# Performance work log

Measured on AMD Instinct MI355X. Metric: run time of the kernel, lower is better.

## Reference

```python
import jax, jax.numpy as jnp
import numpy as np

IN_F, OUT_F = 512, 512
GRID_SIZE, SPLINE_ORDER = 5, 3
K = GRID_SIZE + SPLINE_ORDER  # 8 basis functions
B, S = 8, 1024


def setup_inputs() -> dict:
    key = jax.random.key(0)
    k1, k2, k3, k4, k5 = jax.random.split(key, 5)
    return {
        "x": jax.random.normal(k1, (B, S, IN_F), dtype=jnp.float32),
        "coeff": jax.random.normal(k2, (OUT_F, IN_F, K), dtype=jnp.float32),
        "scale_base": jax.random.normal(k3, (OUT_F, IN_F), dtype=jnp.float32) * 0.1,
        "scale_spline": jax.random.normal(k4, (OUT_F, IN_F), dtype=jnp.float32),
        "base_bias": jax.random.normal(k5, (OUT_F, IN_F), dtype=jnp.float32),
    }


def reference(x, coeff, scale_base, scale_spline, base_bias):
    batch = x.shape[0]
    in_f = x.shape[-1]
    k = coeff.shape[-1]

    xc = jnp.clip(x.reshape(-1, in_f), -1.0, 1.0)      # (N, in)
    base = jax.nn.silu(xc)                              # (N, in)

    # polynomial basis recurrence: b0 = 1, b1 = x, b_i = 2*x*b_{i-1} - 1
    bases = [jnp.ones_like(xc), xc]
    for _ in range(2, k):
        bases.append(2.0 * xc * bases[-1] - 1.0)
    basis = jnp.stack(bases[:k], axis=-1)               # (N, in, K)

    # spline[n,o] = sum_{i,k} scale_spline[o,i]*coeff[o,i,k]*basis[n,i,k]
    w_spline = scale_spline[..., None] * coeff          # (out, in, K)
    spline_term = jnp.einsum('nik,oik->no', basis, w_spline)
    base_term = base @ scale_base.T                     # (N, out)
    out = base_term + spline_term + jnp.sum(base_bias, axis=1)  # (N, out)

    out = out.reshape(batch, -1, base_bias.shape[0])    # (B, S, out)
    if out.shape[-2] == 1:
        out = out[..., 0, :]
    return out
```

## Files before the change

kernel.cpp:

```cpp
#include <hip/hip_runtime.h>
#include <hip/hip_bf16.h>

#define IN_FEAT 512
#define OUT_FEAT 512
#define NTOK 8192
#define KDIM 4096

typedef short bf16x8 __attribute__((ext_vector_type(8)));
typedef float f32x16 __attribute__((ext_vector_type(16)));

static __device__ inline short f2bf(float f) {
    union { float f; unsigned u; } v; v.f = f;
    unsigned u = v.u;
    u += 0x7fffu + ((u >> 16) & 1u);
    return (short)(u >> 16);
}

static __device__ inline unsigned cvtpk(float lo, float hi) {
    unsigned r;
    asm("v_cvt_pk_bf16_f32 %0, %1, %2" : "=v"(r) : "v"(lo), "v"(hi));
    return r;
}

static __device__ inline bf16x8 gen_chunk(float xv) {
    float xc = fminf(fmaxf(xv, -1.f), 1.f);
    float e  = __expf(-xc);
    float bse = xc * __builtin_amdgcn_rcpf(1.f + e);
    float b2 = 2.f * xc * xc - 1.f;
    float b3 = 2.f * xc * b2 - 1.f;
    float b4 = 2.f * xc * b3 - 1.f;
    float b5 = 2.f * xc * b4 - 1.f;
    float b6 = 2.f * xc * b5 - 1.f;
    float b7 = 2.f * xc * b6 - 1.f;
    union { uint4 u; bf16x8 v; } r;
    r.u.x = cvtpk(bse, xc);
    r.u.y = cvtpk(b2, b3);
    r.u.z = cvtpk(b4, b5);
    r.u.w = cvtpk(b6, b7);
    return r.v;
}

static __device__ inline void gload_lds16(const short* g, short* l) {
    __builtin_amdgcn_global_load_lds(
        (const __attribute__((address_space(1))) unsigned int*)g,
        (__attribute__((address_space(3))) unsigned int*)l,
        16, 0, 0);
}

__global__ __launch_bounds__(256) void kan_prep(
    const float* __restrict__ coeff, const float* __restrict__ scale_base,
    const float* __restrict__ scale_spline, const float* __restrict__ base_bias,
    short* __restrict__ Wb, float* __restrict__ bias)
{
    int o = blockIdx.x;
    int tid = threadIdx.x;
    float local = 0.f;
#pragma unroll
    for (int rep = 0; rep < 2; ++rep) {
        int i = tid + rep * 256;
        size_t oi = (size_t)o * IN_FEAT + i;
        const float4* c4 = (const float4*)(coeff + oi * 8);
        float4 ca = c4[0], cb = c4[1];
        float ss = scale_spline[oi];
        float sb = scale_base[oi];
        local += base_bias[oi] + ss * ca.x;
        bf16x8 w;
        w[0] = f2bf(sb);
        w[1] = f2bf(ss * ca.y); w[2] = f2bf(ss * ca.z); w[3] = f2bf(ss * ca.w);
        w[4] = f2bf(ss * cb.x); w[5] = f2bf(ss * cb.y); w[6] = f2bf(ss * cb.z);
        w[7] = f2bf(ss * cb.w);
        *(bf16x8*)(Wb + (size_t)o * KDIM + (size_t)i * 8) = w;
    }
    __shared__ float red[4];
    for (int off = 32; off > 0; off >>= 1) local += __shfl_down(local, off, 64);
    int lane = tid & 63, wv = tid >> 6;
    if (lane == 0) red[wv] = local;
    __syncthreads();
    if (tid == 0) bias[o] = red[0] + red[1] + red[2] + red[3];
}

__global__ __launch_bounds__(256, 2) void kan_gemm16(
    const float* __restrict__ x, const short* __restrict__ Wb,
    const float* __restrict__ bias, float* __restrict__ out)
{
    __shared__ __align__(16) short POOL[20480];
    short* Bs = POOL;

    int tid = threadIdx.x;
    int nb = blockIdx.x & 7;
    int mb = blockIdx.x >> 3;
    int m0 = mb * 128, o0 = nb * 64;

    int lane = tid & 63, wv = tid >> 6;
    int kk = wv;
    int l31 = lane & 31, half = lane >> 5;
    int rm  = l31 & 15;

    f32x16 acc[4][2];
#pragma unroll
    for (int a = 0; a < 4; ++a)
#pragma unroll
        for (int b = 0; b < 2; ++b) acc[a][b] = (f32x16)0.f;

    int rl = lane >> 4, q = lane & 15;
    const short* pB0 = Wb + (size_t)(o0 + wv * 16 +  0 + rl) * KDIM + (size_t)(q ^ ( 0 + rl)) * 8;
    const short* pB1 = Wb + (size_t)(o0 + wv * 16 +  4 + rl) * KDIM + (size_t)(q ^ ( 4 + rl)) * 8;
    const short* pB2 = Wb + (size_t)(o0 + wv * 16 +  8 + rl) * KDIM + (size_t)(q ^ ( 8 + rl)) * 8;
    const short* pB3 = Wb + (size_t)(o0 + wv * 16 + 12 + rl) * KDIM + (size_t)(q ^ (12 + rl)) * 8;

    const float* xp0 = x + (size_t)(m0 + l31) * IN_FEAT + kk * 4;

    int s0 = kk * 4 + half, s1 = s0 + 2;
    int of00 = l31 * 128        + ((s0 ^ rm) * 8);
    int of01 = (32 + l31) * 128 + ((s0 ^ rm) * 8);
    int of10 = l31 * 128        + ((s1 ^ rm) * 8);
    int of11 = (32 + l31) * 128 + ((s1 ^ rm) * 8);

#define MFMA_(A, B, C) __builtin_amdgcn_mfma_f32_32x32x16_bf16(A, B, C, 0, 0, 0)

#define STAGE(BUF, IT, P0, P1, P2, P3)                                        \
    {                                                                         \
        short* bd_ = Bs + (BUF) * 8192 + wv * 2048;                           \
        const size_t bo_ = (size_t)(IT) * 128;                                \
        gload_lds16(pB0 + bo_, bd_);                                          \
        gload_lds16(pB1 + bo_, bd_ + 512);                                    \
        gload_lds16(pB2 + bo_, bd_ + 1024);                                   \
        gload_lds16(pB3 + bo_, bd_ + 1536);                                   \
        const float* xq_ = xp0 + (size_t)(IT) * 16;                           \
        P0 = *(const float4*)(xq_);                                           \
        P1 = *(const float4*)(xq_ + 16384);                                   \
        P2 = *(const float4*)(xq_ + 32768);                                   \
        P3 = *(const float4*)(xq_ + 49152);                                   \
    }

#define COMPUTE(CUR, P0, P1, P2, P3)                                          \
    {                                                                         \
        const short* Bsc_ = Bs + (CUR) * 8192;                                \
        bf16x8 b00 = *(const bf16x8*)(Bsc_ + of00);                           \
        bf16x8 b01 = *(const bf16x8*)(Bsc_ + of01);                           \
        bf16x8 b10 = *(const bf16x8*)(Bsc_ + of10);                           \
        bf16x8 b11 = *(const bf16x8*)(Bsc_ + of11);                           \
        bf16x8 a0 = gen_chunk(half ? (P0).y : (P0).x);                        \
        bf16x8 a1 = gen_chunk(half ? (P1).y : (P1).x);                        \
        bf16x8 a2 = gen_chunk(half ? (P2).y : (P2).x);                        \
        bf16x8 a3 = gen_chunk(half ? (P3).y : (P3).x);                        \
        acc[0][0] = MFMA_(a0, b00, acc[0][0]); acc[0][1] = MFMA_(a0, b01, acc[0][1]); \
        acc[1][0] = MFMA_(a1, b00, acc[1][0]); acc[1][1] = MFMA_(a1, b01, acc[1][1]); \
        acc[2][0] = MFMA_(a2, b00, acc[2][0]); acc[2][1] = MFMA_(a2, b01, acc[2][1]); \
        acc[3][0] = MFMA_(a3, b00, acc[3][0]); acc[3][1] = MFMA_(a3, b01, acc[3][1]); \
        a0 = gen_chunk(half ? (P0).w : (P0).z);                               \
        a1 = gen_chunk(half ? (P1).w : (P1).z);                               \
        a2 = gen_chunk(half ? (P2).w : (P2).z);                               \
        a3 = gen_chunk(half ? (P3).w : (P3).z);                               \
        acc[0][0] = MFMA_(a0, b10, acc[0][0]); acc[0][1] = MFMA_(a0, b11, acc[0][1]); \
        acc[1][0] = MFMA_(a1, b10, acc[1][0]); acc[1][1] = MFMA_(a1, b11, acc[1][1]); \
        acc[2][0] = MFMA_(a2, b10, acc[2][0]); acc[2][1] = MFMA_(a2, b11, acc[2][1]); \
        acc[3][0] = MFMA_(a3, b10, acc[3][0]); acc[3][1] = MFMA_(a3, b11, acc[3][1]); \
    }

    float4 Pa0, Pa1, Pa2, Pa3, Pb0, Pb1, Pb2, Pb3;

    STAGE(0, 0, Pa0, Pa1, Pa2, Pa3);
    for (int j = 0; j < 16; ++j) {
        const int e = 2 * j;
        __syncthreads();
        STAGE(1, e + 1, Pb0, Pb1, Pb2, Pb3);
        COMPUTE(0, Pa0, Pa1, Pa2, Pa3);
        __syncthreads();
        if (e + 1 < 31) STAGE(0, e + 2, Pa0, Pa1, Pa2, Pa3);
        COMPUTE(1, Pb0, Pb1, Pb2, Pb3);
    }
#undef STAGE
#undef COMPUTE
#undef MFMA_

    float* rbuf = (float*)POOL;
#pragma unroll
    for (int p = 0; p < 2; ++p) {
        __syncthreads();
        if (kk >= 2) {
            float* s_ = rbuf + (size_t)(kk - 2) * 4224 + lane * 66;
#pragma unroll
            for (int fm = 0; fm < 2; ++fm)
#pragma unroll
                for (int fn = 0; fn < 2; ++fn)
#pragma unroll
                    for (int r = 0; r < 16; ++r)
                        s_[(fm * 2 + fn) * 16 + r] = acc[2 * p + fm][fn][r];
        }
        __syncthreads();
        if (kk < 2) {
            const float* s_ = rbuf + (size_t)kk * 4224 + lane * 66;
#pragma unroll
            for (int fm = 0; fm < 2; ++fm)
#pragma unroll
                for (int fn = 0; fn < 2; ++fn)
#pragma unroll
                    for (int r = 0; r < 16; ++r)
                        acc[2 * p + fm][fn][r] += s_[(fm * 2 + fn) * 16 + r];
        }
        __syncthreads();
        if (kk == 1) {
            float* s_ = rbuf + lane * 66;
#pragma unroll
            for (int fm = 0; fm < 2; ++fm)
#pragma unroll
                for (int fn = 0; fn < 2; ++fn)
#pragma unroll
                    for (int r = 0; r < 16; ++r)
                        s_[(fm * 2 + fn) * 16 + r] = acc[2 * p + fm][fn][r];
        }
        __syncthreads();
        if (kk == 0) {
            const float* s_ = rbuf + lane * 66;
#pragma unroll
            for (int fn = 0; fn < 2; ++fn) {
                int o = o0 + fn * 32 + l31;
                float bv = bias[o];
#pragma unroll
                for (int fm = 0; fm < 2; ++fm) {
#pragma unroll
                    for (int r = 0; r < 16; ++r) {
                        float v = acc[2 * p + fm][fn][r] + s_[(fm * 2 + fn) * 16 + r] + bv;
                        int token = m0 + (2 * p + fm) * 32 + (r & 3) + 8 * (r >> 2) + 4 * half;
                        out[(size_t)token * OUT_FEAT + o] = v;
                    }
                }
            }
        }
    }
}

extern "C" void kernel_launch(void* const* d_in, const int* in_sizes, int n_in,
                              void* d_out, int out_size, void* d_ws, size_t ws_size,
                              hipStream_t stream) {
    const float* x            = (const float*)d_in[0];
    const float* coeff        = (const float*)d_in[1];
    const float* scale_base   = (const float*)d_in[2];
    const float* scale_spline = (const float*)d_in[3];
    const float* base_bias    = (const float*)d_in[4];
    float* out = (float*)d_out;

    short* Wb   = (short*)d_ws;
    float* bias = (float*)((char*)d_ws + (size_t)OUT_FEAT * KDIM * 2);

    kan_prep<<<OUT_FEAT, 256, 0, stream>>>(coeff, scale_base, scale_spline, base_bias, Wb, bias);
    kan_gemm16<<<(NTOK / 128) * (OUT_FEAT / 64), 256, 0, stream>>>(x, Wb, bias, out);
}
```

Baseline: 127.9 us.

## Double K-step per stage and remap block order for L2 locality

Each pipeline stage now covers 256 K-elements instead of 128. That halves the iterations and the number of __syncthreads barriers, and the B tile in LDS grows to 64x256 with a 32-way XOR swizzle. Each COMPUTE now issues four sub-steps of MFMAs per stage. Block indices are also remapped so that groups of 8 consecutive blocks share N-tiles across M, aiming for better L2 reuse of x or W. The cost is more LDS (64KB) and more registers for prefetched x, which may hurt occupancy at 2 blocks per CU.

```diff
diff --git a/kernel.cpp b/kernel.cpp
--- a/kernel.cpp
+++ b/kernel.cpp
@@ -79,22 +79,23 @@
     if (tid == 0) bias[o] = red[0] + red[1] + red[2] + red[3];
 }
 
-__global__ __launch_bounds__(256, 2) void kan_gemm16(
+__global__ __launch_bounds__(256, 2) void kan_gemm17(
     const float* __restrict__ x, const short* __restrict__ Wb,
     const float* __restrict__ bias, float* __restrict__ out)
 {
-    __shared__ __align__(16) short POOL[20480];
+    __shared__ __align__(16) short POOL[32768];
     short* Bs = POOL;
 
     int tid = threadIdx.x;
-    int nb = blockIdx.x & 7;
-    int mb = blockIdx.x >> 3;
+    int bid = blockIdx.x;
+    int j8 = bid & 7, t = bid >> 3;
+    int mb = j8 * 8 + (t & 7);
+    int nb = t >> 3;
     int m0 = mb * 128, o0 = nb * 64;
 
     int lane = tid & 63, wv = tid >> 6;
     int kk = wv;
     int l31 = lane & 31, half = lane >> 5;
-    int rm  = l31 & 15;
 
     f32x16 acc[4][2];
 #pragma unroll
@@ -102,76 +103,78 @@
 #pragma unroll
         for (int b = 0; b < 2; ++b) acc[a][b] = (f32x16)0.f;
 
-    int rl = lane >> 4, q = lane & 15;
-    const short* pB0 = Wb + (size_t)(o0 + wv * 16 +  0 + rl) * KDIM + (size_t)(q ^ ( 0 + rl)) * 8;
-    const short* pB1 = Wb + (size_t)(o0 + wv * 16 +  4 + rl) * KDIM + (size_t)(q ^ ( 4 + rl)) * 8;
-    const short* pB2 = Wb + (size_t)(o0 + wv * 16 +  8 + rl) * KDIM + (size_t)(q ^ ( 8 + rl)) * 8;
-    const short* pB3 = Wb + (size_t)(o0 + wv * 16 + 12 + rl) * KDIM + (size_t)(q ^ (12 + rl)) * 8;
-
-    const float* xp0 = x + (size_t)(m0 + l31) * IN_FEAT + kk * 4;
-
-    int s0 = kk * 4 + half, s1 = s0 + 2;
-    int of00 = l31 * 128        + ((s0 ^ rm) * 8);
-    int of01 = (32 + l31) * 128 + ((s0 ^ rm) * 8);
-    int of10 = l31 * 128        + ((s1 ^ rm) * 8);
-    int of11 = (32 + l31) * 128 + ((s1 ^ rm) * 8);
+    int rl2 = lane >> 5, q32 = lane & 31;
+    const short* pB[8];
+#pragma unroll
+    for (int c = 0; c < 8; ++c) {
+        int row = wv * 16 + c * 2 + rl2;
+        int g = q32 ^ (row & 31);
+        pB[c] = Wb + (size_t)(o0 + row) * KDIM + (size_t)g * 8;
+    }
+    int bd0 = wv * 16 * 256;
+
+    const float* xp0 = x + (size_t)(m0 + l31) * IN_FEAT + kk * 8;
+
+    int ofr[4];
+#pragma unroll
+    for (int j = 0; j < 4; ++j)
+        ofr[j] = l31 * 256 + (((kk * 8 + 2 * j + half) ^ l31) * 8);
 
 #define MFMA_(A, B, C) __builtin_amdgcn_mfma_f32_32x32x16_bf16(A, B, C, 0, 0, 0)
 
-#define STAGE(BUF, IT, P0, P1, P2, P3)                                        \
+#define GENSEL(Qa, Qb, J) ((J) == 0 ? (half ? (Qa).y : (Qa).x)                \
+                         : (J) == 1 ? (half ? (Qa).w : (Qa).z)                \
+                         : (J) == 2 ? (half ? (Qb).y : (Qb).x)                \
+                                    : (half ? (Qb).w : (Qb).z))
+
+#define STAGE(BUF, IT, Q0a, Q0b, Q1a, Q1b, Q2a, Q2b, Q3a, Q3b)                \
     {                                                                         \
-        short* bd_ = Bs + (BUF) * 8192 + wv * 2048;                           \
-        const size_t bo_ = (size_t)(IT) * 128;                                \
-        gload_lds16(pB0 + bo_, bd_);                                          \
-        gload_lds16(pB1 + bo_, bd_ + 512);                                    \
-        gload_lds16(pB2 + bo_, bd_ + 1024);                                   \
-        gload_lds16(pB3 + bo_, bd_ + 1536);                                   \
-        const float* xq_ = xp0 + (size_t)(IT) * 16;                           \
-        P0 = *(const float4*)(xq_);                                           \
-        P1 = *(const float4*)(xq_ + 16384);                                   \
-        P2 = *(const float4*)(xq_ + 32768);                                   \
-        P3 = *(const float4*)(xq_ + 49152);                                   \
-    }
-
-#define COMPUTE(CUR, P0, P1, P2, P3)                                          \
+        short* bd_ = Bs + (BUF) * 16384 + bd0;                                \
+        const size_t bo_ = (size_t)(IT) * 256;                                \
+        _Pragma("unroll")                                                     \
+        for (int c_ = 0; c_ < 8; ++c_)                                        \
+            gload_lds16(pB[c_] + bo_, bd_ + c_ * 512);                        \
+        const float* xq_ = xp0 + (size_t)(IT) * 32;                           \
+        Q0a = *(const float4*)(xq_);          Q0b = *(const float4*)(xq_ + 4);          \
+        Q1a = *(const float4*)(xq_ + 16384);  Q1b = *(const float4*)(xq_ + 16388);      \
+        Q2a = *(const float4*)(xq_ + 32768);  Q2b = *(const float4*)(xq_ + 32772);      \
+        Q3a = *(const float4*)(xq_ + 49152);  Q3b = *(const float4*)(xq_ + 49156);      \
+    }
+
+#define COMPUTE(CUR, Q0a, Q0b, Q1a, Q1b, Q2a, Q2b, Q3a, Q3b)                  \
     {                                                                         \
-        const short* Bsc_ = Bs + (CUR) * 8192;                                \
-        bf16x8 b00 = *(const bf16x8*)(Bsc_ + of00);                           \
-        bf16x8 b01 = *(const bf16x8*)(Bsc_ + of01);                           \
-        bf16x8 b10 = *(const bf16x8*)(Bsc_ + of10);                           \
-        bf16x8 b11 = *(const bf16x8*)(Bsc_ + of11);                           \
-        bf16x8 a0 = gen_chunk(half ? (P0).y : (P0).x);                        \
-        bf16x8 a1 = gen_chunk(half ? (P1).y : (P1).x);                        \
-        bf16x8 a2 = gen_chunk(half ? (P2).y : (P2).x);                        \
-        bf16x8 a3 = gen_chunk(half ? (P3).y : (P3).x);                        \
-        acc[0][0] = MFMA_(a0, b00, acc[0][0]); acc[0][1] = MFMA_(a0, b01, acc[0][1]); \
-        acc[1][0] = MFMA_(a1, b00, acc[1][0]); acc[1][1] = MFMA_(a1, b01, acc[1][1]); \
-        acc[2][0] = MFMA_(a2, b00, acc[2][0]); acc[2][1] = MFMA_(a2, b01, acc[2][1]); \
-        acc[3][0] = MFMA_(a3, b00, acc[3][0]); acc[3][1] = MFMA_(a3, b01, acc[3][1]); \
-        a0 = gen_chunk(half ? (P0).w : (P0).z);                               \
-        a1 = gen_chunk(half ? (P1).w : (P1).z);                               \
-        a2 = gen_chunk(half ? (P2).w : (P2).z);                               \
-        a3 = gen_chunk(half ? (P3).w : (P3).z);                               \
-        acc[0][0] = MFMA_(a0, b10, acc[0][0]); acc[0][1] = MFMA_(a0, b11, acc[0][1]); \
-        acc[1][0] = MFMA_(a1, b10, acc[1][0]); acc[1][1] = MFMA_(a1, b11, acc[1][1]); \
-        acc[2][0] = MFMA_(a2, b10, acc[2][0]); acc[2][1] = MFMA_(a2, b11, acc[2][1]); \
-        acc[3][0] = MFMA_(a3, b10, acc[3][0]); acc[3][1] = MFMA_(a3, b11, acc[3][1]); \
-    }
-
-    float4 Pa0, Pa1, Pa2, Pa3, Pb0, Pb1, Pb2, Pb3;
-
-    STAGE(0, 0, Pa0, Pa1, Pa2, Pa3);
-    for (int j = 0; j < 16; ++j) {
-        const int e = 2 * j;
-        __syncthreads();
-        STAGE(1, e + 1, Pb0, Pb1, Pb2, Pb3);
-        COMPUTE(0, Pa0, Pa1, Pa2, Pa3);
-        __syncthreads();
-        if (e + 1 < 31) STAGE(0, e + 2, Pa0, Pa1, Pa2, Pa3);
-        COMPUTE(1, Pb0, Pb1, Pb2, Pb3);
+        const short* Bc_ = Bs + (CUR) * 16384;                                \
+        _Pragma("unroll")                                                     \
+        for (int j_ = 0; j_ < 4; ++j_) {                                      \
+            bf16x8 b0_ = *(const bf16x8*)(Bc_ + ofr[j_]);                     \
+            bf16x8 b1_ = *(const bf16x8*)(Bc_ + ofr[j_] + 8192);              \
+            bf16x8 a0_ = gen_chunk(GENSEL(Q0a, Q0b, j_));                     \
+            bf16x8 a1_ = gen_chunk(GENSEL(Q1a, Q1b, j_));                     \
+            bf16x8 a2_ = gen_chunk(GENSEL(Q2a, Q2b, j_));                     \
+            bf16x8 a3_ = gen_chunk(GENSEL(Q3a, Q3b, j_));                     \
+            acc[0][0] = MFMA_(a0_, b0_, acc[0][0]); acc[0][1] = MFMA_(a0_, b1_, acc[0][1]); \
+            acc[1][0] = MFMA_(a1_, b0_, acc[1][0]); acc[1][1] = MFMA_(a1_, b1_, acc[1][1]); \
+            acc[2][0] = MFMA_(a2_, b0_, acc[2][0]); acc[2][1] = MFMA_(a2_, b1_, acc[2][1]); \
+            acc[3][0] = MFMA_(a3_, b0_, acc[3][0]); acc[3][1] = MFMA_(a3_, b1_, acc[3][1]); \
+        }                                                                     \
+    }
+
+    float4 A0a, A0b, A1a, A1b, A2a, A2b, A3a, A3b;
+    float4 B0a, B0b, B1a, B1b, B2a, B2b, B3a, B3b;
+
+    STAGE(0, 0, A0a, A0b, A1a, A1b, A2a, A2b, A3a, A3b);
+    for (int jj = 0; jj < 8; ++jj) {
+        __syncthreads();
+        STAGE(1, 2 * jj + 1, B0a, B0b, B1a, B1b, B2a, B2b, B3a, B3b);
+        COMPUTE(0, A0a, A0b, A1a, A1b, A2a, A2b, A3a, A3b);
+        __syncthreads();
+        if (jj < 7)
+            STAGE(0, 2 * jj + 2, A0a, A0b, A1a, A1b, A2a, A2b, A3a, A3b);
+        COMPUTE(1, B0a, B0b, B1a, B1b, B2a, B2b, B3a, B3b);
     }
 #undef STAGE
 #undef COMPUTE
+#undef GENSEL
 #undef MFMA_
 
     float* rbuf = (float*)POOL;
@@ -245,5 +248,5 @@
     float* bias = (float*)((char*)d_ws + (size_t)OUT_FEAT * KDIM * 2);
 
     kan_prep<<<OUT_FEAT, 256, 0, stream>>>(coeff, scale_base, scale_spline, base_bias, Wb, bias);
-    kan_gemm16<<<(NTOK / 128) * (OUT_FEAT / 64), 256, 0, stream>>>(x, Wb, bias, out);
-}
+    kan_gemm17<<<(NTOK / 128) * (OUT_FEAT / 64), 256, 0, stream>>>(x, Wb, bias, out);
+}
```

Result: no change. 126.5 us (-1.1%).

## Split GEMM block into 8 waves with phased barrier pipeline and setprio

Applied to the files above, without the earlier changes.

Moves the spline GEMM from 256 to 512 threads per block. Waves are split across two M halves and four K slices, so each wave holds half the accumulators, and the launch bound rises to 4 blocks per CU. The main loop becomes a finer phased pipeline: LDS and global prefetches for the next stage are issued alongside the MFMAs, guarded by raw s_barrier, s_setprio and explicit vmcnt waits. Blocks are remapped so that groups share x rows in cache, and the reduction scratch layout switches to a lane-strided form that avoids bank conflicts. The trade-off is more barriers per tile and correctness that depends on the hand-placed waitcnt counts.

```diff
diff --git a/kernel.cpp b/kernel.cpp
--- a/kernel.cpp
+++ b/kernel.cpp
@@ -79,140 +79,178 @@
     if (tid == 0) bias[o] = red[0] + red[1] + red[2] + red[3];
 }
 
-__global__ __launch_bounds__(256, 2) void kan_gemm16(
+__global__ __launch_bounds__(512, 4) void kan_gemm18(
     const float* __restrict__ x, const short* __restrict__ Wb,
     const float* __restrict__ bias, float* __restrict__ out)
 {
-    __shared__ __align__(16) short POOL[20480];
+    __shared__ __align__(16) short POOL[16384];
     short* Bs = POOL;
 
     int tid = threadIdx.x;
-    int nb = blockIdx.x & 7;
-    int mb = blockIdx.x >> 3;
+    int bid = blockIdx.x;
+    int j8 = bid & 7, t5 = bid >> 3;
+    int mb = j8 * 8 + (t5 & 7);
+    int nb = t5 >> 3;
     int m0 = mb * 128, o0 = nb * 64;
 
     int lane = tid & 63, wv = tid >> 6;
-    int kk = wv;
+    int wm = wv & 1, kk = wv >> 1;
     int l31 = lane & 31, half = lane >> 5;
     int rm  = l31 & 15;
 
-    f32x16 acc[4][2];
-#pragma unroll
-    for (int a = 0; a < 4; ++a)
+    f32x16 acc[2][2];
+#pragma unroll
+    for (int a = 0; a < 2; ++a)
 #pragma unroll
         for (int b = 0; b < 2; ++b) acc[a][b] = (f32x16)0.f;
 
     int rl = lane >> 4, q = lane & 15;
-    const short* pB0 = Wb + (size_t)(o0 + wv * 16 +  0 + rl) * KDIM + (size_t)(q ^ ( 0 + rl)) * 8;
-    const short* pB1 = Wb + (size_t)(o0 + wv * 16 +  4 + rl) * KDIM + (size_t)(q ^ ( 4 + rl)) * 8;
-    const short* pB2 = Wb + (size_t)(o0 + wv * 16 +  8 + rl) * KDIM + (size_t)(q ^ ( 8 + rl)) * 8;
-    const short* pB3 = Wb + (size_t)(o0 + wv * 16 + 12 + rl) * KDIM + (size_t)(q ^ (12 + rl)) * 8;
-
-    const float* xp0 = x + (size_t)(m0 + l31) * IN_FEAT + kk * 4;
-
-    int s0 = kk * 4 + half, s1 = s0 + 2;
-    int of00 = l31 * 128        + ((s0 ^ rm) * 8);
-    int of01 = (32 + l31) * 128 + ((s0 ^ rm) * 8);
-    int of10 = l31 * 128        + ((s1 ^ rm) * 8);
-    int of11 = (32 + l31) * 128 + ((s1 ^ rm) * 8);
+    int ra = wv * 8 + rl, rb = ra + 4;
+    const short* pBa = Wb + (size_t)(o0 + ra) * KDIM + (size_t)(q ^ (ra & 15)) * 8;
+    const short* pBb = Wb + (size_t)(o0 + rb) * KDIM + (size_t)(q ^ (rb & 15)) * 8;
+    int bda = (wv * 8) * 128;
+    int bdb = bda + 512;
+
+    const float* xp0 = x + (size_t)(m0 + wm * 64 + l31) * IN_FEAT + kk * 4;
+
+    int of0 = l31 * 128 + (((kk * 4 + 0 + half) ^ rm) * 8);
+    int of1 = l31 * 128 + (((kk * 4 + 2 + half) ^ rm) * 8);
 
 #define MFMA_(A, B, C) __builtin_amdgcn_mfma_f32_32x32x16_bf16(A, B, C, 0, 0, 0)
 
-#define STAGE(BUF, IT, P0, P1, P2, P3)                                        \
-    {                                                                         \
-        short* bd_ = Bs + (BUF) * 8192 + wv * 2048;                           \
-        const size_t bo_ = (size_t)(IT) * 128;                                \
-        gload_lds16(pB0 + bo_, bd_);                                          \
-        gload_lds16(pB1 + bo_, bd_ + 512);                                    \
-        gload_lds16(pB2 + bo_, bd_ + 1024);                                   \
-        gload_lds16(pB3 + bo_, bd_ + 1536);                                   \
-        const float* xq_ = xp0 + (size_t)(IT) * 16;                           \
-        P0 = *(const float4*)(xq_);                                           \
-        P1 = *(const float4*)(xq_ + 16384);                                   \
-        P2 = *(const float4*)(xq_ + 32768);                                   \
-        P3 = *(const float4*)(xq_ + 49152);                                   \
-    }
-
-#define COMPUTE(CUR, P0, P1, P2, P3)                                          \
-    {                                                                         \
-        const short* Bsc_ = Bs + (CUR) * 8192;                                \
-        bf16x8 b00 = *(const bf16x8*)(Bsc_ + of00);                           \
-        bf16x8 b01 = *(const bf16x8*)(Bsc_ + of01);                           \
-        bf16x8 b10 = *(const bf16x8*)(Bsc_ + of10);                           \
-        bf16x8 b11 = *(const bf16x8*)(Bsc_ + of11);                           \
-        bf16x8 a0 = gen_chunk(half ? (P0).y : (P0).x);                        \
-        bf16x8 a1 = gen_chunk(half ? (P1).y : (P1).x);                        \
-        bf16x8 a2 = gen_chunk(half ? (P2).y : (P2).x);                        \
-        bf16x8 a3 = gen_chunk(half ? (P3).y : (P3).x);                        \
-        acc[0][0] = MFMA_(a0, b00, acc[0][0]); acc[0][1] = MFMA_(a0, b01, acc[0][1]); \
-        acc[1][0] = MFMA_(a1, b00, acc[1][0]); acc[1][1] = MFMA_(a1, b01, acc[1][1]); \
-        acc[2][0] = MFMA_(a2, b00, acc[2][0]); acc[2][1] = MFMA_(a2, b01, acc[2][1]); \
-        acc[3][0] = MFMA_(a3, b00, acc[3][0]); acc[3][1] = MFMA_(a3, b01, acc[3][1]); \
-        a0 = gen_chunk(half ? (P0).w : (P0).z);                               \
-        a1 = gen_chunk(half ? (P1).w : (P1).z);                               \
-        a2 = gen_chunk(half ? (P2).w : (P2).z);                               \
-        a3 = gen_chunk(half ? (P3).w : (P3).z);                               \
-        acc[0][0] = MFMA_(a0, b10, acc[0][0]); acc[0][1] = MFMA_(a0, b11, acc[0][1]); \
-        acc[1][0] = MFMA_(a1, b10, acc[1][0]); acc[1][1] = MFMA_(a1, b11, acc[1][1]); \
-        acc[2][0] = MFMA_(a2, b10, acc[2][0]); acc[2][1] = MFMA_(a2, b11, acc[2][1]); \
-        acc[3][0] = MFMA_(a3, b10, acc[3][0]); acc[3][1] = MFMA_(a3, b11, acc[3][1]); \
-    }
-
-    float4 Pa0, Pa1, Pa2, Pa3, Pb0, Pb1, Pb2, Pb3;
-
-    STAGE(0, 0, Pa0, Pa1, Pa2, Pa3);
-    for (int j = 0; j < 16; ++j) {
-        const int e = 2 * j;
-        __syncthreads();
-        STAGE(1, e + 1, Pb0, Pb1, Pb2, Pb3);
-        COMPUTE(0, Pa0, Pa1, Pa2, Pa3);
-        __syncthreads();
-        if (e + 1 < 31) STAGE(0, e + 2, Pa0, Pa1, Pa2, Pa3);
-        COMPUTE(1, Pb0, Pb1, Pb2, Pb3);
-    }
-#undef STAGE
-#undef COMPUTE
+#define PHASE0(CUR, IT1, PC0, PC1)                                            \
+    {                                                                         \
+        const short* Bc_ = Bs + (CUR) * 8192;                                 \
+        bf16x8 b0_ = *(const bf16x8*)(Bc_ + of0);                             \
+        bf16x8 b1_ = *(const bf16x8*)(Bc_ + of0 + 4096);                      \
+        short* bd_ = Bs + ((CUR) ^ 1) * 8192;                                 \
+        gload_lds16(pBa + (size_t)(IT1) * 128, bd_ + bda);                    \
+        gload_lds16(pBb + (size_t)(IT1) * 128, bd_ + bdb);                    \
+        bf16x8 a0_ = gen_chunk(half ? (PC0).y : (PC0).x);                     \
+        bf16x8 a1_ = gen_chunk(half ? (PC1).y : (PC1).x);                     \
+        __builtin_amdgcn_s_barrier();                                         \
+        __builtin_amdgcn_s_setprio(1);                                        \
+        acc[0][0] = MFMA_(a0_, b0_, acc[0][0]);                               \
+        acc[0][1] = MFMA_(a0_, b1_, acc[0][1]);                               \
+        acc[1][0] = MFMA_(a1_, b0_, acc[1][0]);                               \
+        acc[1][1] = MFMA_(a1_, b1_, acc[1][1]);                               \
+        __builtin_amdgcn_s_setprio(0);                                        \
+        __builtin_amdgcn_s_barrier();                                         \
+    }
+
+#define PHASE1(CUR, IT1, PC0, PC1, PN0, PN1)                                  \
+    {                                                                         \
+        const short* Bc_ = Bs + (CUR) * 8192;                                 \
+        bf16x8 b0_ = *(const bf16x8*)(Bc_ + of1);                             \
+        bf16x8 b1_ = *(const bf16x8*)(Bc_ + of1 + 4096);                      \
+        const float* xq_ = xp0 + (size_t)(IT1) * 16;                          \
+        PN0 = *(const float4*)(xq_);                                          \
+        PN1 = *(const float4*)(xq_ + 16384);                                  \
+        bf16x8 a0_ = gen_chunk(half ? (PC0).w : (PC0).z);                     \
+        bf16x8 a1_ = gen_chunk(half ? (PC1).w : (PC1).z);                     \
+        __builtin_amdgcn_s_barrier();                                         \
+        __builtin_amdgcn_s_setprio(1);                                        \
+        acc[0][0] = MFMA_(a0_, b0_, acc[0][0]);                               \
+        acc[0][1] = MFMA_(a0_, b1_, acc[0][1]);                               \
+        acc[1][0] = MFMA_(a1_, b0_, acc[1][0]);                               \
+        acc[1][1] = MFMA_(a1_, b1_, acc[1][1]);                               \
+        __builtin_amdgcn_s_setprio(0);                                        \
+        asm volatile("s_waitcnt vmcnt(2)" ::: "memory");                      \
+        __builtin_amdgcn_s_barrier();                                         \
+    }
+
+#define PHASE0T(CUR, PC0, PC1)                                                \
+    {                                                                         \
+        const short* Bc_ = Bs + (CUR) * 8192;                                 \
+        bf16x8 b0_ = *(const bf16x8*)(Bc_ + of0);                             \
+        bf16x8 b1_ = *(const bf16x8*)(Bc_ + of0 + 4096);                      \
+        bf16x8 a0_ = gen_chunk(half ? (PC0).y : (PC0).x);                     \
+        bf16x8 a1_ = gen_chunk(half ? (PC1).y : (PC1).x);                     \
+        __builtin_amdgcn_s_barrier();                                         \
+        acc[0][0] = MFMA_(a0_, b0_, acc[0][0]);                               \
+        acc[0][1] = MFMA_(a0_, b1_, acc[0][1]);                               \
+        acc[1][0] = MFMA_(a1_, b0_, acc[1][0]);                               \
+        acc[1][1] = MFMA_(a1_, b1_, acc[1][1]);                               \
+        __builtin_amdgcn_s_barrier();                                         \
+    }
+#define PHASE1T(CUR, PC0, PC1)                                                \
+    {                                                                         \
+        const short* Bc_ = Bs + (CUR) * 8192;                                 \
+        bf16x8 b0_ = *(const bf16x8*)(Bc_ + of1);                             \
+        bf16x8 b1_ = *(const bf16x8*)(Bc_ + of1 + 4096);                      \
+        bf16x8 a0_ = gen_chunk(half ? (PC0).w : (PC0).z);                     \
+        bf16x8 a1_ = gen_chunk(half ? (PC1).w : (PC1).z);                     \
+        __builtin_amdgcn_s_barrier();                                         \
+        acc[0][0] = MFMA_(a0_, b0_, acc[0][0]);                               \
+        acc[0][1] = MFMA_(a0_, b1_, acc[0][1]);                               \
+        acc[1][0] = MFMA_(a1_, b0_, acc[1][0]);                               \
+        acc[1][1] = MFMA_(a1_, b1_, acc[1][1]);                               \
+    }
+
+    float4 Pa0, Pa1, Pb0, Pb1;
+
+    gload_lds16(pBa, Bs + bda);
+    gload_lds16(pBb, Bs + bdb);
+    Pa0 = *(const float4*)(xp0);
+    Pa1 = *(const float4*)(xp0 + 16384);
+    asm volatile("s_waitcnt vmcnt(2)" ::: "memory");
+    __builtin_amdgcn_s_barrier();
+
+    for (int j = 0; j < 15; ++j) {
+        PHASE0(0, 2 * j + 1, Pa0, Pa1);
+        PHASE1(0, 2 * j + 1, Pa0, Pa1, Pb0, Pb1);
+        PHASE0(1, 2 * j + 2, Pb0, Pb1);
+        PHASE1(1, 2 * j + 2, Pb0, Pb1, Pa0, Pa1);
+    }
+    PHASE0(0, 31, Pa0, Pa1);
+    PHASE1(0, 31, Pa0, Pa1, Pb0, Pb1);
+    PHASE0T(1, Pb0, Pb1);
+    PHASE1T(1, Pb0, Pb1);
+#undef PHASE0
+#undef PHASE1
+#undef PHASE0T
+#undef PHASE1T
 #undef MFMA_
 
     float* rbuf = (float*)POOL;
 #pragma unroll
     for (int p = 0; p < 2; ++p) {
         __syncthreads();
-        if (kk >= 2) {
-            float* s_ = rbuf + (size_t)(kk - 2) * 4224 + lane * 66;
+        if (wm == p && kk >= 2) {
+            float* s_ = rbuf + (size_t)(kk - 2) * 4096 + lane;
 #pragma unroll
             for (int fm = 0; fm < 2; ++fm)
 #pragma unroll
                 for (int fn = 0; fn < 2; ++fn)
 #pragma unroll
                     for (int r = 0; r < 16; ++r)
-                        s_[(fm * 2 + fn) * 16 + r] = acc[2 * p + fm][fn][r];
-        }
-        __syncthreads();
-        if (kk < 2) {
-            const float* s_ = rbuf + (size_t)kk * 4224 + lane * 66;
+                        s_[((fm * 2 + fn) * 16 + r) * 64] = acc[fm][fn][r];
+        }
+        __syncthreads();
+        if (wm == p && kk < 2) {
+            const float* s_ = rbuf + (size_t)kk * 4096 + lane;
 #pragma unroll
             for (int fm = 0; fm < 2; ++fm)
 #pragma unroll
                 for (int fn = 0; fn < 2; ++fn)
 #pragma unroll
                     for (int r = 0; r < 16; ++r)
-                        acc[2 * p + fm][fn][r] += s_[(fm * 2 + fn) * 16 + r];
-        }
-        __syncthreads();
-        if (kk == 1) {
-            float* s_ = rbuf + lane * 66;
+                        acc[fm][fn][r] += s_[((fm * 2 + fn) * 16 + r) * 64];
+        }
+        __syncthreads();
+        if (wm == p && kk == 1) {
+            float* s_ = rbuf + lane;
 #pragma unroll
             for (int fm = 0; fm < 2; ++fm)
 #pragma unroll
                 for (int fn = 0; fn < 2; ++fn)
 #pragma unroll
                     for (int r = 0; r < 16; ++r)
-                        s_[(fm * 2 + fn) * 16 + r] = acc[2 * p + fm][fn][r];
-        }
-        __syncthreads();
-        if (kk == 0) {
-            const float* s_ = rbuf + lane * 66;
+                        s_[((fm * 2 + fn) * 16 + r) * 64] = acc[fm][fn][r];
+        }
+        __syncthreads();
+        if (wm == p && kk == 0) {
+            const float* s_ = rbuf + lane;
 #pragma unroll
             for (int fn = 0; fn < 2; ++fn) {
                 int o = o0 + fn * 32 + l31;
@@ -221,8 +259,8 @@
                 for (int fm = 0; fm < 2; ++fm) {
 #pragma unroll
                     for (int r = 0; r < 16; ++r) {
-                        float v = acc[2 * p + fm][fn][r] + s_[(fm * 2 + fn) * 16 + r] + bv;
-                        int token = m0 + (2 * p + fm) * 32 + (r & 3) + 8 * (r >> 2) + 4 * half;
+                        float v = acc[fm][fn][r] + s_[((fm * 2 + fn) * 16 + r) * 64] + bv;
+                        int token = m0 + wm * 64 + fm * 32 + (r & 3) + 8 * (r >> 2) + 4 * half;
                         out[(size_t)token * OUT_FEAT + o] = v;
                     }
                 }
@@ -245,5 +283,5 @@
     float* bias = (float*)((char*)d_ws + (size_t)OUT_FEAT * KDIM * 2);
 
     kan_prep<<<OUT_FEAT, 256, 0, stream>>>(coeff, scale_base, scale_spline, base_bias, Wb, bias);
-    kan_gemm16<<<(NTOK / 128) * (OUT_FEAT / 64), 256, 0, stream>>>(x, Wb, bias, out);
-}
+    kan_gemm18<<<(NTOK / 128) * (OUT_FEAT / 64), 512, 0, stream>>>(x, Wb, bias, out);
+}
```

Result: slower. 131.3 us (+2.7%).
